# Kernel tuning notes

Hardware: AMD Instinct MI355X
Metric: run time of the kernel (lower is better)

The kernel has to match this reference:

```python
import jax, jax.numpy as jnp
import numpy as np

# Model constants (match init_kwargs / torchcde conventions)
B = 1024        # batch
L = 128         # number of spline knots (grid_points = 0..L-1)
C_IN = 8        # input_channels
HID = 64        # hidden_channels
MLP_H = 128     # CDEFunc hidden width
INIT_H = 20     # initial-network hidden width


def setup_inputs() -> dict:
    key = jax.random.key(0)
    ks = jax.random.split(key, 9)
    # cubic spline coeffs: (B, L-1, 4*C_IN) laid out as [a, b, c, d] per interval
    coeffs = jax.random.normal(ks[0], (B, L - 1, 4 * C_IN), dtype=jnp.float32) * 0.1
    # initial network: C_IN -> 20 -> HID (ReLU, then Tanh)
    Wi1 = jax.random.normal(ks[1], (C_IN, INIT_H), dtype=jnp.float32) / np.sqrt(C_IN)
    bi1 = jnp.zeros((INIT_H,), jnp.float32)
    Wi2 = jax.random.normal(ks[2], (INIT_H, HID), dtype=jnp.float32) / np.sqrt(INIT_H)
    bi2 = jnp.zeros((HID,), jnp.float32)
    # CDE vector field: (HID+1) -> 128 -> C_IN*HID (ReLU, then Tanh)
    W1 = jax.random.normal(ks[3], (HID + 1, MLP_H), dtype=jnp.float32) / np.sqrt(HID + 1)
    b1 = jnp.zeros((MLP_H,), jnp.float32)
    W2 = jax.random.normal(ks[4], (MLP_H, C_IN * HID), dtype=jnp.float32) / np.sqrt(MLP_H)
    b2 = jnp.zeros((C_IN * HID,), jnp.float32)
    return {"coeffs": coeffs, "Wi1": Wi1, "bi1": bi1, "Wi2": Wi2, "bi2": bi2,
            "W1": W1, "b1": b1, "W2": W2, "b2": b2}


def reference(coeffs, Wi1, bi1, Wi2, bi2, W1, b1, W2, b2):
    Lm1 = coeffs.shape[1]
    # a,b,c,d: each (B, L-1, C_IN). X(t) = a + b*f + c*f^2 + d*f^3 on interval idx,
    # dX/dt = b + 2c*f + 3d*f^2, with f = t - idx (torchcde CubicSpline convention).
    a, b, c, d = jnp.split(coeffs, 4, axis=-1)

    def dXdt(t):
        idx = jnp.clip(jnp.floor(t).astype(jnp.int32), 0, Lm1 - 1)
        fr = t - idx
        return b[:, idx] + 2.0 * c[:, idx] * fr + 3.0 * d[:, idx] * fr * fr  # (B, C_IN)

    def cde_func(t, z):
        # FFN([HID+1, 128, C_IN*HID], ReLU hidden, Tanh output) on concat(t, z)
        tz = jnp.concatenate([jnp.full((z.shape[0], 1), t, z.dtype), z], axis=1)
        h = jax.nn.relu(tz @ W1 + b1)
        return jnp.tanh(h @ W2 + b2).reshape(z.shape[0], HID, C_IN)  # (B, HID, C_IN)

    def vf(t, z):
        # dz/dt = f(t,z) @ dX/dt
        return jnp.einsum('bhc,bc->bh', cde_func(t, z), dXdt(t))

    # z0 = initial(X(t0)); X(0) = a at interval 0 with frac 0
    X0 = a[:, 0]
    z0 = jnp.tanh(jax.nn.relu(X0 @ Wi1 + bi1) @ Wi2 + bi2)  # (B, HID)

    def rk4_step(z, i):
        t = i.astype(z.dtype)
        k1 = vf(t, z)
        k2 = vf(t + 0.5, z + 0.5 * k1)
        k3 = vf(t + 0.5, z + 0.5 * k2)
        k4 = vf(t + 1.0, z + k3)
        z_new = z + (k1 + 2.0 * k2 + 2.0 * k3 + k4) / 6.0
        return z_new, z_new

    _, zs = jax.lax.scan(rk4_step, z0, jnp.arange(Lm1))  # (L-1, B, HID)
    # z evaluated at all grid points, like cdeint(t=X.grid_points): (B, L, HID)
    return jnp.concatenate([z0[None], zs], axis=0).transpose(1, 0, 2)
```

## Files before the change

### kernel.cpp

```cpp
#include <hip/hip_runtime.h>
#include <stdint.h>

#define LM1  127
#define NTHR 1024

typedef _Float16 half8_t __attribute__((ext_vector_type(8)));
typedef float    f32x4   __attribute__((ext_vector_type(4)));
typedef float    f32x2   __attribute__((ext_vector_type(2)));

__device__ __forceinline__ float fast_tanh(float x) {
  float e = __expf(2.0f * x);
  return 1.0f - 2.0f * __builtin_amdgcn_rcpf(e + 1.0f);
}

__global__ void __launch_bounds__(NTHR, 4) cde_kernel(
    const float* __restrict__ coeffs,
    const float* __restrict__ Wi1, const float* __restrict__ bi1,
    const float* __restrict__ Wi2, const float* __restrict__ bi2,
    const float* __restrict__ W1,  const float* __restrict__ b1,
    const float* __restrict__ W2,  const float* __restrict__ b2,
    float* __restrict__ out)
{
  __shared__ _Float16 zsb[1024];
  __shared__ _Float16 hA [2048];
  __shared__ float    fwb[16][144];
  __shared__ float    gds[2][3][4][8];

  const int t    = threadIdx.x;
  const int lane = t & 63;
  const int w    = t >> 6;
  const int l15  = lane & 15;
  const int lq   = lane >> 4;
  const int r    = lane & 3;
  const int row0 = blockIdx.x * 4;

  for (int u = t; u < 512;  u += NTHR) ((uint32_t*)zsb)[u] = 0u;
  for (int u = t; u < 1024; u += NTHR) ((uint32_t*)hA)[u]  = 0u;

  half8_t bB[2] = {};
  float w1t_c = 0.f, b1_c = 0.f;
  if (w < 8) {
    #pragma unroll
    for (int kt = 0; kt < 2; ++kt)
      #pragma unroll
      for (int j = 0; j < 8; ++j)
        bB[kt][j] = (_Float16)W1[(1 + kt * 32 + lq * 8 + j) * 128 + w * 16 + l15];
    w1t_c = W1[w * 16 + l15];
    b1_c  = b1[w * 16 + l15];
  }

  half8_t bf[2][4];
  #pragma unroll
  for (int nt = 0; nt < 2; ++nt)
    #pragma unroll
    for (int kt = 0; kt < 4; ++kt)
      #pragma unroll
      for (int j = 0; j < 8; ++j)
        bf[nt][kt][j] =
            (_Float16)W2[(kt * 32 + lq * 8 + j) * 512 + w * 32 + nt * 16 + l15];

  const int q    = lane >> 4;
  const int hxlk = (lane >> 2) & 3;
  const int hxk  = w * 4 + hxlk;
  const float b2r0 = b2[hxk * 8 + 2 * q];
  const float b2r1 = b2[hxk * 8 + 2 * q + 1];

  const int hx = w * 4 + (lane >> 2);
  _Float16* zwp;
  {
    const int kh = hx >> 5, lqw = (hx >> 3) & 3, j = hx & 7;
    zwp = &zsb[8 * (kh * 64 + lqw * 16 + r) + j];
  }
  _Float16* hwp;
  {
    const int col = 16 * w + l15;
    const int ktw = (col >> 5) & 3, lqw2 = (col >> 3) & 3, j2 = col & 7;
    hwp = &hA[8 * (ktw * 64 + lqw2 * 16) + j2];
  }
  float* const fsp = &fwb[w][36 * (l15 >> 3) + 4 * (l15 & 7)];
  const float* const frp = &fwb[w][36 * hxlk + 8 * q + r];

  float z = 0.0f;
  if (lane < 16) {
    const float* cb = coeffs + (size_t)(row0 + r) * (LM1 * 32);
    float x0[8];
    #pragma unroll
    for (int c = 0; c < 8; ++c) x0[c] = cb[c];
    float acc = bi2[hx];
    for (int j = 0; j < 20; ++j) {
      float u = bi1[j];
      #pragma unroll
      for (int c = 0; c < 8; ++c) u += x0[c] * Wi1[c * 20 + j];
      acc += fmaxf(u, 0.0f) * Wi2[j * 64 + hx];
    }
    z = fast_tanh(acc);
    out[(size_t)(row0 + r) * 8192 + hx] = z;
  }

  const int rg = (t >> 3) & 3, cg = t & 7;
  const float* cbp = coeffs + (size_t)(row0 + rg) * (LM1 * 32);
  float pb = 0.f, pc = 0.f, pd = 0.f, pbn = 0.f;
  if (t < 32) { pb = cbp[8 + cg]; pc = cbp[16 + cg]; pd = cbp[24 + cg]; pbn = cbp[40 + cg]; }

  __syncthreads();

  for (int i = 0; i < LM1; ++i) {
    if (t < 32) {
      gds[i & 1][0][rg][cg] = pb;
      gds[i & 1][1][rg][cg] = pb + pc + 0.75f * pd;
      gds[i & 1][2][rg][cg] = (i < LM1 - 1) ? pbn : fmaf(3.0f, pd, fmaf(2.0f, pc, pb));
      if (i + 1 < LM1) {
        const float* nb = cbp + (size_t)(i + 1) * 32;
        pb = nb[8 + cg]; pc = nb[16 + cg]; pd = nb[24 + cg];
        pbn = (i + 2 < LM1) ? nb[40 + cg] : 0.0f;
      }
    }

    float ksum = 0.0f, kprev = 0.0f;
    #pragma unroll
    for (int s = 0; s < 4; ++s) {
      const float coef = (s == 0) ? 0.0f : (s == 3) ? 1.0f : 0.5f;
      const float ts   = (float)i + ((s == 0) ? 0.0f : (s == 3) ? 1.0f : 0.5f);
      const int   gi   = (s == 0) ? 0 : (s == 3) ? 2 : 1;

      if (lane < 16) *zwp = (_Float16)(z + coef * kprev);
      __syncthreads();

      if (w < 8) {
        const half8_t a0 = *(const half8_t*)(zsb + 8 * lane);
        const half8_t a1 = *(const half8_t*)(zsb + 512 + 8 * lane);
        f32x4 hd = {0.f, 0.f, 0.f, 0.f};
        hd = __builtin_amdgcn_mfma_f32_16x16x32_f16(a0, bB[0], hd, 0, 0, 0);
        hd = __builtin_amdgcn_mfma_f32_16x16x32_f16(a1, bB[1], hd, 0, 0, 0);
        if (lane < 16) {
          const float hb = fmaf(ts, w1t_c, b1_c);
          hwp[0]  = (_Float16)fmaxf(hd.x + hb, 0.0f);
          hwp[8]  = (_Float16)fmaxf(hd.y + hb, 0.0f);
          hwp[16] = (_Float16)fmaxf(hd.z + hb, 0.0f);
          hwp[24] = (_Float16)fmaxf(hd.w + hb, 0.0f);
        }
      }
      __syncthreads();

      {
        half8_t ha[4];
        #pragma unroll
        for (int kt = 0; kt < 4; ++kt)
          ha[kt] = *(const half8_t*)(hA + 512 * kt + 8 * lane);
        f32x4 d0 = {0.f, 0.f, 0.f, 0.f}, d1 = d0;
        #pragma unroll
        for (int kt = 0; kt < 4; ++kt) {
          d0 = __builtin_amdgcn_mfma_f32_16x16x32_f16(ha[kt], bf[0][kt], d0, 0, 0, 0);
          d1 = __builtin_amdgcn_mfma_f32_16x16x32_f16(ha[kt], bf[1][kt], d1, 0, 0, 0);
        }
        if (lane < 16) {
          *(f32x4*)(fsp)      = d0;
          *(f32x4*)(fsp + 72) = d1;
        }
      }
      asm volatile("s_waitcnt lgkmcnt(0)" ::: "memory");

      {
        const float v0 = frp[0], v1 = frp[4];
        const f32x2 gv = *(const f32x2*)&gds[i & 1][gi][r][2 * q];
        float kcv = fast_tanh(v0 + b2r0) * gv.x + fast_tanh(v1 + b2r1) * gv.y;
        kcv += __shfl_xor(kcv, 16, 64);
        kcv += __shfl_xor(kcv, 32, 64);
        kprev = kcv;
        ksum += ((s == 1 || s == 2) ? 2.0f : 1.0f) * kcv;
      }
    }
    if (lane < 16) {
      z += ksum * (1.0f / 6.0f);
      out[(size_t)(row0 + r) * 8192 + (size_t)(i + 1) * 64 + hx] = z;
    }
  }
}

extern "C" void kernel_launch(void* const* d_in, const int* in_sizes, int n_in,
                              void* d_out, int out_size, void* d_ws, size_t ws_size,
                              hipStream_t stream) {
  const float* coeffs = (const float*)d_in[0];
  const float* Wi1    = (const float*)d_in[1];
  const float* bi1    = (const float*)d_in[2];
  const float* Wi2    = (const float*)d_in[3];
  const float* bi2    = (const float*)d_in[4];
  const float* W1     = (const float*)d_in[5];
  const float* b1     = (const float*)d_in[6];
  const float* W2     = (const float*)d_in[7];
  const float* b2     = (const float*)d_in[8];
  float* out          = (float*)d_out;
  (void)in_sizes; (void)n_in; (void)out_size; (void)d_ws; (void)ws_size;
  cde_kernel<<<256, NTHR, 0, stream>>>(coeffs, Wi1, bi1, Wi2, bi2,
                                       W1, b1, W2, b2, out);
}
```

Before: 539.5 us.

## Split work so waves 8-15 run layer-1 MFMA and waves 0-7 run layer-2

Restructures the per-block wave assignment. The first-layer MFMA moves to waves 8-15, and the second-layer matmul plus the tanh/dX reduction is concentrated on waves 0-7, each now covering 64 output columns with four accumulators. The final reduction drops one cross-lane shuffle, and the coefficient staging moves to wave 15. The aim is to cut per-step work on the critical path and reduce shuffles, at the cost of more registers per wave and unbalanced work across waves.

```diff
diff --git a/kernel.cpp b/kernel.cpp
--- a/kernel.cpp
+++ b/kernel.cpp
@@ -6,7 +6,6 @@
 
 typedef _Float16 half8_t __attribute__((ext_vector_type(8)));
 typedef float    f32x4   __attribute__((ext_vector_type(4)));
-typedef float    f32x2   __attribute__((ext_vector_type(2)));
 
 __device__ __forceinline__ float fast_tanh(float x) {
   float e = __expf(2.0f * x);
@@ -21,68 +20,72 @@
     const float* __restrict__ W2,  const float* __restrict__ b2,
     float* __restrict__ out)
 {
-  __shared__ _Float16 zsb[1024];
-  __shared__ _Float16 hA [2048];
-  __shared__ float    fwb[16][144];
-  __shared__ float    gds[2][3][4][8];
+  __shared__ __align__(16) _Float16 zsb[1024];
+  __shared__ __align__(16) _Float16 hA [2048];
+  __shared__ __align__(16) float    fwb[8][288];
+  __shared__ __align__(16) float    gds[2][3][4][8];
 
   const int t    = threadIdx.x;
   const int lane = t & 63;
   const int w    = t >> 6;
   const int l15  = lane & 15;
   const int lq   = lane >> 4;
-  const int r    = lane & 3;
   const int row0 = blockIdx.x * 4;
+  const int wc   = w & 7;
 
   for (int u = t; u < 512;  u += NTHR) ((uint32_t*)zsb)[u] = 0u;
   for (int u = t; u < 1024; u += NTHR) ((uint32_t*)hA)[u]  = 0u;
 
   half8_t bB[2] = {};
   float w1t_c = 0.f, b1_c = 0.f;
-  if (w < 8) {
+  _Float16* hwp = &hA[0];
+  if (w >= 8) {
+    const int wb = w - 8;
     #pragma unroll
     for (int kt = 0; kt < 2; ++kt)
       #pragma unroll
       for (int j = 0; j < 8; ++j)
-        bB[kt][j] = (_Float16)W1[(1 + kt * 32 + lq * 8 + j) * 128 + w * 16 + l15];
-    w1t_c = W1[w * 16 + l15];
-    b1_c  = b1[w * 16 + l15];
-  }
-
-  half8_t bf[2][4];
-  #pragma unroll
-  for (int nt = 0; nt < 2; ++nt)
-    #pragma unroll
-    for (int kt = 0; kt < 4; ++kt)
+        bB[kt][j] = (_Float16)W1[(1 + kt * 32 + lq * 8 + j) * 128 + wb * 16 + l15];
+    w1t_c = W1[wb * 16 + l15];
+    b1_c  = b1[wb * 16 + l15];
+    const int col = 16 * wb + l15;
+    const int ktw = (col >> 5) & 3, lqw2 = (col >> 3) & 3, j2 = col & 7;
+    hwp = &hA[8 * (ktw * 64 + lqw2 * 16) + j2];
+  }
+
+  half8_t bf[4][4] = {};
+  if (w < 8) {
+    #pragma unroll
+    for (int nt = 0; nt < 4; ++nt)
       #pragma unroll
-      for (int j = 0; j < 8; ++j)
-        bf[nt][kt][j] =
-            (_Float16)W2[(kt * 32 + lq * 8 + j) * 512 + w * 32 + nt * 16 + l15];
-
-  const int q    = lane >> 4;
-  const int hxlk = (lane >> 2) & 3;
-  const int hxk  = w * 4 + hxlk;
-  const float b2r0 = b2[hxk * 8 + 2 * q];
-  const float b2r1 = b2[hxk * 8 + 2 * q + 1];
-
-  const int hx = w * 4 + (lane >> 2);
+      for (int kt = 0; kt < 4; ++kt)
+        #pragma unroll
+        for (int j = 0; j < 8; ++j)
+          bf[nt][kt][j] =
+              (_Float16)W2[(kt * 32 + lq * 8 + j) * 512 + w * 64 + nt * 16 + l15];
+  }
+
+  const int r_ = lane & 3;
+  const int hh = (lane >> 2) & 7;
+  const int cp = lane >> 5;
+  float b2c0 = 0.f, b2c1 = 0.f, b2c2 = 0.f, b2c3 = 0.f;
+  if (w < 8) {
+    const float* bp = b2 + w * 64 + hh * 8 + cp * 4;
+    b2c0 = bp[0]; b2c1 = bp[1]; b2c2 = bp[2]; b2c3 = bp[3];
+  }
+  const int frbase = 36 * hh + 16 * cp + r_;
+  const int hx = 8 * wc + hh;
+
   _Float16* zwp;
   {
-    const int kh = hx >> 5, lqw = (hx >> 3) & 3, j = hx & 7;
-    zwp = &zsb[8 * (kh * 64 + lqw * 16 + r) + j];
-  }
-  _Float16* hwp;
-  {
-    const int col = 16 * w + l15;
-    const int ktw = (col >> 5) & 3, lqw2 = (col >> 3) & 3, j2 = col & 7;
-    hwp = &hA[8 * (ktw * 64 + lqw2 * 16) + j2];
-  }
-  float* const fsp = &fwb[w][36 * (l15 >> 3) + 4 * (l15 & 7)];
-  const float* const frp = &fwb[w][36 * hxlk + 8 * q + r];
+    const int kh = hx >> 5, lqw = (hx >> 3) & 3, jj = hx & 7;
+    zwp = &zsb[8 * (kh * 64 + lqw * 16 + r_) + jj];
+  }
+  float* const fsp = &fwb[wc][36 * (l15 >> 3) + 4 * (l15 & 7)];
 
   float z = 0.0f;
-  if (lane < 16) {
-    const float* cb = coeffs + (size_t)(row0 + r) * (LM1 * 32);
+  if (w < 8 && lane < 32) {
+    const float* cb = coeffs + (size_t)(row0 + r_) * (LM1 * 32);
     float x0[8];
     #pragma unroll
     for (int c = 0; c < 8; ++c) x0[c] = cb[c];
@@ -94,18 +97,19 @@
       acc += fmaxf(u, 0.0f) * Wi2[j * 64 + hx];
     }
     z = fast_tanh(acc);
-    out[(size_t)(row0 + r) * 8192 + hx] = z;
-  }
-
-  const int rg = (t >> 3) & 3, cg = t & 7;
+    out[(size_t)(row0 + r_) * 8192 + hx] = z;
+  }
+
+  const int rg = (lane >> 3) & 3, cg = lane & 7;
   const float* cbp = coeffs + (size_t)(row0 + rg) * (LM1 * 32);
   float pb = 0.f, pc = 0.f, pd = 0.f, pbn = 0.f;
-  if (t < 32) { pb = cbp[8 + cg]; pc = cbp[16 + cg]; pd = cbp[24 + cg]; pbn = cbp[40 + cg]; }
+  const bool stg = (w == 15) && (lane < 32);
+  if (stg) { pb = cbp[8 + cg]; pc = cbp[16 + cg]; pd = cbp[24 + cg]; pbn = cbp[40 + cg]; }
 
   __syncthreads();
 
   for (int i = 0; i < LM1; ++i) {
-    if (t < 32) {
+    if (stg) {
       gds[i & 1][0][rg][cg] = pb;
       gds[i & 1][1][rg][cg] = pb + pc + 0.75f * pd;
       gds[i & 1][2][rg][cg] = (i < LM1 - 1) ? pbn : fmaf(3.0f, pd, fmaf(2.0f, pc, pb));
@@ -123,10 +127,10 @@
       const float ts   = (float)i + ((s == 0) ? 0.0f : (s == 3) ? 1.0f : 0.5f);
       const int   gi   = (s == 0) ? 0 : (s == 3) ? 2 : 1;
 
-      if (lane < 16) *zwp = (_Float16)(z + coef * kprev);
+      if (w < 8 && lane < 32) *zwp = (_Float16)(z + coef * kprev);
       __syncthreads();
 
-      if (w < 8) {
+      if (w >= 8) {
         const half8_t a0 = *(const half8_t*)(zsb + 8 * lane);
         const half8_t a1 = *(const half8_t*)(zsb + 512 + 8 * lane);
         f32x4 hd = {0.f, 0.f, 0.f, 0.f};
@@ -142,37 +146,40 @@
       }
       __syncthreads();
 
-      {
+      if (w < 8) {
         half8_t ha[4];
         #pragma unroll
         for (int kt = 0; kt < 4; ++kt)
           ha[kt] = *(const half8_t*)(hA + 512 * kt + 8 * lane);
-        f32x4 d0 = {0.f, 0.f, 0.f, 0.f}, d1 = d0;
+        f32x4 d0 = {0.f, 0.f, 0.f, 0.f}, d1 = d0, d2 = d0, d3 = d0;
         #pragma unroll
         for (int kt = 0; kt < 4; ++kt) {
           d0 = __builtin_amdgcn_mfma_f32_16x16x32_f16(ha[kt], bf[0][kt], d0, 0, 0, 0);
           d1 = __builtin_amdgcn_mfma_f32_16x16x32_f16(ha[kt], bf[1][kt], d1, 0, 0, 0);
+          d2 = __builtin_amdgcn_mfma_f32_16x16x32_f16(ha[kt], bf[2][kt], d2, 0, 0, 0);
+          d3 = __builtin_amdgcn_mfma_f32_16x16x32_f16(ha[kt], bf[3][kt], d3, 0, 0, 0);
         }
         if (lane < 16) {
-          *(f32x4*)(fsp)      = d0;
-          *(f32x4*)(fsp + 72) = d1;
+          *(f32x4*)(fsp)       = d0;
+          *(f32x4*)(fsp + 72)  = d1;
+          *(f32x4*)(fsp + 144) = d2;
+          *(f32x4*)(fsp + 216) = d3;
         }
-      }
-      asm volatile("s_waitcnt lgkmcnt(0)" ::: "memory");
-
-      {
-        const float v0 = frp[0], v1 = frp[4];
-        const f32x2 gv = *(const f32x2*)&gds[i & 1][gi][r][2 * q];
-        float kcv = fast_tanh(v0 + b2r0) * gv.x + fast_tanh(v1 + b2r1) * gv.y;
-        kcv += __shfl_xor(kcv, 16, 64);
+        asm volatile("s_waitcnt lgkmcnt(0)" ::: "memory");
+
+        const float* fb = &fwb[wc][frbase];
+        const float v0 = fb[0], v1 = fb[4], v2 = fb[8], v3 = fb[12];
+        const f32x4 gv = *(const f32x4*)&gds[i & 1][gi][r_][4 * cp];
+        float kcv = fast_tanh(v0 + b2c0) * gv.x + fast_tanh(v1 + b2c1) * gv.y
+                  + fast_tanh(v2 + b2c2) * gv.z + fast_tanh(v3 + b2c3) * gv.w;
         kcv += __shfl_xor(kcv, 32, 64);
         kprev = kcv;
         ksum += ((s == 1 || s == 2) ? 2.0f : 1.0f) * kcv;
       }
     }
-    if (lane < 16) {
+    if (w < 8 && lane < 32) {
       z += ksum * (1.0f / 6.0f);
-      out[(size_t)(row0 + r) * 8192 + (size_t)(i + 1) * 64 + hx] = z;
+      out[(size_t)(row0 + r_) * 8192 + (size_t)(i + 1) * 64 + hx] = z;
     }
   }
 }
```

New measurement: 567.3 us. 5.2% more time.
